# Kernel tuning notes

Hardware: AMD Instinct MI355X
Metric: run time of the kernel (lower is better)

The kernel has to match this reference:

```python
import jax, jax.numpy as jnp
import numpy as np

B, T, D, H, C = 128, 256, 256, 1024, 10


def setup_inputs() -> dict:
    key = jax.random.key(0)
    ks = jax.random.split(key, 11)
    std = 1.0 / T  # matches nn.init.normal_(std=1/seq_length)
    inp = {
        'x':   jax.random.normal(ks[0], (B, T, D), dtype=jnp.float32),
        'Wfx': jax.random.normal(ks[1], (D, H), dtype=jnp.float32) * std,
        'Wix': jax.random.normal(ks[2], (D, H), dtype=jnp.float32) * std,
        'Wgx': jax.random.normal(ks[3], (D, H), dtype=jnp.float32) * std,
        'Wox': jax.random.normal(ks[4], (D, H), dtype=jnp.float32) * std,
        'Wfh': jax.random.normal(ks[5], (H, H), dtype=jnp.float32) * std,
        'Wih': jax.random.normal(ks[6], (H, H), dtype=jnp.float32) * std,
        'Wgh': jax.random.normal(ks[7], (H, H), dtype=jnp.float32) * std,
        'Woh': jax.random.normal(ks[8], (H, H), dtype=jnp.float32) * std,
        'bf':  jnp.zeros((H,), jnp.float32),
        'bi':  jnp.zeros((H,), jnp.float32),
        'bg':  jnp.zeros((H,), jnp.float32),
        'bo':  jnp.zeros((H,), jnp.float32),
        'Wph': jax.random.normal(ks[9], (H, C), dtype=jnp.float32) * std,
        'bp':  jnp.zeros((C,), jnp.float32),
    }
    return inp


def reference(x, Wfx, Wix, Wgx, Wox, Wfh, Wih, Wgh, Woh, bf, bi, bg, bo, Wph, bp):
    b, t, d = x.shape
    h = Wfh.shape[0]
    # Fuse the 4 input-side and 4 hidden-side matmuls into two big GEMMs per step
    Wx = jnp.concatenate([Wfx, Wix, Wgx, Wox], axis=1)  # [D, 4H]
    Wh = jnp.concatenate([Wfh, Wih, Wgh, Woh], axis=1)  # [H, 4H]
    bb = jnp.concatenate([bf, bi, bg, bo])              # [4H]

    # Precompute all input projections in one batched GEMM: [T, B, 4H]
    xg = jnp.einsum('btd,dk->tbk', x, Wx) + bb

    def step(carry, xgt):
        hs, cs = carry
        gates = xgt + hs @ Wh  # [B, 4H]
        f = jax.nn.sigmoid(gates[:, 0 * h:1 * h])
        i = jax.nn.sigmoid(gates[:, 1 * h:2 * h])
        g = jnp.tanh(gates[:, 2 * h:3 * h])
        o = jax.nn.sigmoid(gates[:, 3 * h:4 * h])
        cs = g * i + cs * f
        hs = jnp.tanh(cs) * o
        return (hs, cs), None

    h0 = jnp.zeros((b, h), x.dtype)
    c0 = jnp.zeros((b, h), x.dtype)
    (hT, _), _ = jax.lax.scan(step, (h0, c0), xg)
    return hT @ Wph + bp
```

## Files before the change

### kernel.cpp

```cpp
#include <hip/hip_runtime.h>
#include <math.h>


#define BB 128
#define TT 256
#define DD 256
#define HH 1024
#define NKT 40
#define KHT 20
#define PFA 4
#define PFB 5

typedef __bf16 bf16x8 __attribute__((ext_vector_type(8)));
typedef float  f32x4  __attribute__((ext_vector_type(4)));
typedef unsigned short u16;
typedef u16 u16x8 __attribute__((ext_vector_type(8)));

__device__ __forceinline__ u16 f2bf(float f){
  unsigned u = __builtin_bit_cast(unsigned, f);
  u += 0x7fffu + ((u >> 16) & 1u);
  return (u16)(u >> 16);
}
__device__ __forceinline__ float bf2f(u16 b){
  unsigned u = ((unsigned)b) << 16;
  return __builtin_bit_cast(float, u);
}
__device__ __forceinline__ float sigm(float x){
  return 1.f / (1.f + __expf(-x));
}
__device__ __forceinline__ float tanh_fast(float x){
  return 2.f / (1.f + __expf(-2.f * x)) - 1.f;
}
__device__ __forceinline__ int swzb(int slot){
  return slot ^ ((slot >> 6) & 7) ^ (((slot >> 4) & 3) << 1);
}

__global__ void prep_wpack(const float* __restrict__ Wfx, const float* __restrict__ Wix,
                           const float* __restrict__ Wgx, const float* __restrict__ Wox,
                           const float* __restrict__ Wfh, const float* __restrict__ Wih,
                           const float* __restrict__ Wgh, const float* __restrict__ Woh,
                           u16* __restrict__ Wpack){
  int id = blockIdx.x * 256 + threadIdx.x;
  int lane = id & 63;
  int kt = (id >> 6) % NKT;
  int ct = id / (64 * NKT);
  int col = ct * 16 + (lane & 15);
  int g = col >> 10, n = col & 1023;
  int kbase = kt * 32 + (lane >> 4) * 8;
  const float* Wx = (g==0) ? Wfx : (g==1) ? Wix : (g==2) ? Wgx : Wox;
  const float* Wh = (g==0) ? Wfh : (g==1) ? Wih : (g==2) ? Wgh : Woh;
  u16x8 v;
  #pragma unroll
  for (int j = 0; j < 8; ++j){
    int k = kbase + j;
    float f = (k < DD) ? Wx[k * HH + n] : Wh[(k - DD) * HH + n];
    v[j] = f2bf(f);
  }
  *(u16x8*)(Wpack + (size_t)id * 8) = v;
}

__global__ void prep_xT(const float* __restrict__ x, u16* __restrict__ xT){
  int id = blockIdx.x * 256 + threadIdx.x;
  int t = id >> 12;
  int b = (id >> 5) & 127;
  int d0 = (id & 31) * 8;
  const float* src = x + ((size_t)b * TT + t) * DD + d0;
  u16x8 v;
  #pragma unroll
  for (int j = 0; j < 8; ++j) v[j] = f2bf(src[j]);
  *(u16x8*)(xT + (size_t)id * 8) = v;
}

__global__ __launch_bounds__(512) void lstm_step(
    const u16* __restrict__ xTt,
    const u16* __restrict__ Wpack,
    const u16* __restrict__ hin,
    u16* __restrict__ hout,
    float* __restrict__ cbuf,
    const float* __restrict__ bfv, const float* __restrict__ biv,
    const float* __restrict__ bgv, const float* __restrict__ bov){
  __shared__ u16x8 As4[NKT * 64];
  __shared__ float gLds[16][132];
  __shared__ float pLds[16][132];
  const int tid = threadIdx.x;
  const int n0 = blockIdx.x * 32;
  const int m0 = blockIdx.y * 16;

  const int crow = tid >> 5, cnn = tid & 31;
  const int gi = (m0 + crow) * HH + n0 + cnn;
  const float cprev = cbuf[gi];

  const int w = tid >> 6, lane = tid & 63, cr = lane & 15, q4 = lane >> 4;
  const int g  = w & 3;
  const int kh = w >> 2;
  const int ktBeg = kh * KHT;

  const size_t ct0 = (size_t)(g * 64 + blockIdx.x * 2);
  const u16x8* Wp = (const u16x8*)Wpack;
  const u16x8* wq0 = Wp + ct0 * NKT * 64 + lane;
  const u16x8* wq1 = wq0 + NKT * 64;

  u16x8 aP[PFA], b0P[PFB], b1P[PFB];
  #pragma unroll
  for (int i = 0; i < PFB; ++i){
    b0P[i] = wq0[(size_t)(ktBeg + i) * 64];
    b1P[i] = wq1[(size_t)(ktBeg + i) * 64];
  }

  #pragma unroll
  for (int it = 0; it < 10; ++it){
    int ch = tid + it * 256;
    ch = tid + it * 512;
    if (it >= 5) break;
    int m = ch / 160;
    int k0 = (ch - m * 160) * 8;
    const u16* src = (k0 < DD) ? (xTt + (m0 + m) * DD + k0)
                               : (hin + (m0 + m) * HH + (k0 - DD));
    u16x8 val = *(const u16x8*)src;
    int kt = k0 >> 5, q = (k0 >> 3) & 3;
    As4[swzb(kt * 64 + 16 * q + m)] = val;
  }
  __syncthreads();

  #pragma unroll
  for (int i = 0; i < PFA; ++i) aP[i] = As4[swzb((ktBeg + i) * 64 + lane)];

  f32x4 acc0 = {0.f, 0.f, 0.f, 0.f}, acc1 = {0.f, 0.f, 0.f, 0.f};
  #pragma unroll
  for (int kt = 0; kt < KHT; ++kt){
    u16x8 ac = aP[kt % PFA], b0 = b0P[kt % PFB], b1 = b1P[kt % PFB];
    if (kt + PFA < KHT)
      aP[kt % PFA] = As4[swzb((ktBeg + kt + PFA) * 64 + lane)];
    if (kt + PFB < KHT){
      b0P[kt % PFB] = wq0[(size_t)(ktBeg + kt + PFB) * 64];
      b1P[kt % PFB] = wq1[(size_t)(ktBeg + kt + PFB) * 64];
    }
    acc0 = __builtin_amdgcn_mfma_f32_16x16x32_bf16(__builtin_bit_cast(bf16x8, ac),
             __builtin_bit_cast(bf16x8, b0), acc0, 0, 0, 0);
    acc1 = __builtin_amdgcn_mfma_f32_16x16x32_bf16(__builtin_bit_cast(bf16x8, ac),
             __builtin_bit_cast(bf16x8, b1), acc1, 0, 0, 0);
  }

  if (kh){
    #pragma unroll
    for (int r = 0; r < 4; ++r){
      pLds[q4 * 4 + r][g * 32 + cr]      = acc0[r];
      pLds[q4 * 4 + r][g * 32 + 16 + cr] = acc1[r];
    }
  }
  __syncthreads();
  if (!kh){
    const float* bptr = (g==0) ? bfv : (g==1) ? biv : (g==2) ? bgv : bov;
    float bias0 = bptr[n0 + cr], bias1 = bptr[n0 + 16 + cr];
    #pragma unroll
    for (int r = 0; r < 4; ++r){
      gLds[q4 * 4 + r][g * 32 + cr] =
          acc0[r] + pLds[q4 * 4 + r][g * 32 + cr] + bias0;
      gLds[q4 * 4 + r][g * 32 + 16 + cr] =
          acc1[r] + pLds[q4 * 4 + r][g * 32 + 16 + cr] + bias1;
    }
  }
  __syncthreads();

  {
    float fp = gLds[crow][cnn],      ip = gLds[crow][32 + cnn];
    float gp = gLds[crow][64 + cnn], op = gLds[crow][96 + cnn];
    float fs = sigm(fp);
    float is = sigm(ip);
    float gs = tanh_fast(gp);
    float os = sigm(op);
    float cn = gs * is + cprev * fs;
    cbuf[gi] = cn;
    hout[gi] = f2bf(tanh_fast(cn) * os);
  }
}

__global__ void final_proj(const u16* __restrict__ h, const float* __restrict__ Wph,
                           const float* __restrict__ bp, float* __restrict__ out){
  __shared__ float red[10][256];
  int b = blockIdx.x, tid = threadIdx.x;
  float p[10];
  #pragma unroll
  for (int c = 0; c < 10; ++c) p[c] = 0.f;
  for (int k = tid; k < HH; k += 256){
    float hv = bf2f(h[b * HH + k]);
    const float* wr = Wph + (size_t)k * 10;
    #pragma unroll
    for (int c = 0; c < 10; ++c) p[c] += hv * wr[c];
  }
  #pragma unroll
  for (int c = 0; c < 10; ++c) red[c][tid] = p[c];
  __syncthreads();
  for (int s = 128; s > 0; s >>= 1){
    if (tid < s){
      #pragma unroll
      for (int c = 0; c < 10; ++c) red[c][tid] += red[c][tid + s];
    }
    __syncthreads();
  }
  if (tid < 10) out[b * 10 + tid] = red[tid][0] + bp[tid];
}

extern "C" void kernel_launch(void* const* d_in, const int* in_sizes, int n_in,
                              void* d_out, int out_size, void* d_ws, size_t ws_size,
                              hipStream_t stream){
  (void)in_sizes; (void)n_in; (void)out_size; (void)ws_size;
  const float* x   = (const float*)d_in[0];
  const float* Wfx = (const float*)d_in[1];
  const float* Wix = (const float*)d_in[2];
  const float* Wgx = (const float*)d_in[3];
  const float* Wox = (const float*)d_in[4];
  const float* Wfh = (const float*)d_in[5];
  const float* Wih = (const float*)d_in[6];
  const float* Wgh = (const float*)d_in[7];
  const float* Woh = (const float*)d_in[8];
  const float* bfv = (const float*)d_in[9];
  const float* biv = (const float*)d_in[10];
  const float* bgv = (const float*)d_in[11];
  const float* bov = (const float*)d_in[12];
  const float* Wph = (const float*)d_in[13];
  const float* bp  = (const float*)d_in[14];

  char* ws = (char*)d_ws;
  u16*  Wpack = (u16*)ws;
  u16*  xT    = (u16*)(ws + 10485760);
  u16*  h0    = (u16*)(ws + 27262976);
  u16*  h1    = (u16*)(ws + 27525120);
  float* cb   = (float*)(ws + 27787264);

  prep_wpack<<<2560, 256, 0, stream>>>(Wfx, Wix, Wgx, Wox, Wfh, Wih, Wgh, Woh, Wpack);
  prep_xT<<<4096, 256, 0, stream>>>(x, xT);
  hipMemsetAsync(h0, 0, 262144, stream);
  hipMemsetAsync(cb, 0, 524288, stream);

  for (int t = 0; t < TT; ++t){
    const u16* hin  = (t & 1) ? h1 : h0;
    u16*       hout = (t & 1) ? h0 : h1;
    lstm_step<<<dim3(32, 8), 512, 0, stream>>>(xT + (size_t)t * BB * DD, Wpack,
                                               hin, hout, cb, bfv, biv, bgv, bov);
  }
  final_proj<<<128, 256, 0, stream>>>(h0, Wph, bp, (float*)d_out);
}
```

Before: 1.951 ms.

## Double batch rows per block to reuse weight fragments across two MFMA tiles

Each step block now processes 32 batch rows instead of 16, loading each weight fragment once and using it for two MFMA tiles, which halves the grid size. The split-K reduction writes both halves to separate LDS buffers and sums them in the gate epilogue, dropping one barrier. The weight prefetch depth is raised. This cuts global weight traffic per step but leaves fewer blocks to cover the GPU's compute units and raises per-block LDS and register use.

```diff
diff --git a/kernel.cpp b/kernel.cpp
--- a/kernel.cpp
+++ b/kernel.cpp
@@ -9,7 +9,7 @@
 #define NKT 40
 #define KHT 20
 #define PFA 4
-#define PFB 5
+#define PFB 8
 
 typedef __bf16 bf16x8 __attribute__((ext_vector_type(8)));
 typedef float  f32x4  __attribute__((ext_vector_type(4)));
@@ -71,7 +71,7 @@
   *(u16x8*)(xT + (size_t)id * 8) = v;
 }
 
-__global__ __launch_bounds__(512) void lstm_step(
+__global__ __launch_bounds__(512) void lstm_step3(
     const u16* __restrict__ xTt,
     const u16* __restrict__ Wpack,
     const u16* __restrict__ hin,
@@ -79,16 +79,20 @@
     float* __restrict__ cbuf,
     const float* __restrict__ bfv, const float* __restrict__ biv,
     const float* __restrict__ bgv, const float* __restrict__ bov){
-  __shared__ u16x8 As4[NKT * 64];
-  __shared__ float gLds[16][132];
-  __shared__ float pLds[16][132];
+  __shared__ u16x8 AsLo[NKT * 64];
+  __shared__ u16x8 AsHi[NKT * 64];
+  __shared__ float pLds0[32][132];
+  __shared__ float pLds1[32][132];
   const int tid = threadIdx.x;
   const int n0 = blockIdx.x * 32;
-  const int m0 = blockIdx.y * 16;
-
-  const int crow = tid >> 5, cnn = tid & 31;
-  const int gi = (m0 + crow) * HH + n0 + cnn;
-  const float cprev = cbuf[gi];
+  const int m0 = blockIdx.y * 32;
+
+  const int crow0 = tid >> 5,        cnn0 = tid & 31;
+  const int crow1 = (tid + 512) >> 5, cnn1 = cnn0;
+  const int gi0 = (m0 + crow0) * HH + n0 + cnn0;
+  const int gi1 = (m0 + crow1) * HH + n0 + cnn1;
+  const float cprev0 = cbuf[gi0];
+  const float cprev1 = cbuf[gi1];
 
   const int w = tid >> 6, lane = tid & 63, cr = lane & 15, q4 = lane >> 4;
   const int g  = w & 3;
@@ -100,7 +104,7 @@
   const u16x8* wq0 = Wp + ct0 * NKT * 64 + lane;
   const u16x8* wq1 = wq0 + NKT * 64;
 
-  u16x8 aP[PFA], b0P[PFB], b1P[PFB];
+  u16x8 b0P[PFB], b1P[PFB];
   #pragma unroll
   for (int i = 0; i < PFB; ++i){
     b0P[i] = wq0[(size_t)(ktBeg + i) * 64];
@@ -108,70 +112,98 @@
   }
 
   #pragma unroll
-  for (int it = 0; it < 10; ++it){
-    int ch = tid + it * 256;
-    ch = tid + it * 512;
-    if (it >= 5) break;
+  for (int it = 0; it < 5; ++it){
+    int ch = tid + it * 512;
     int m = ch / 160;
     int k0 = (ch - m * 160) * 8;
     const u16* src = (k0 < DD) ? (xTt + (m0 + m) * DD + k0)
                                : (hin + (m0 + m) * HH + (k0 - DD));
     u16x8 val = *(const u16x8*)src;
     int kt = k0 >> 5, q = (k0 >> 3) & 3;
-    As4[swzb(kt * 64 + 16 * q + m)] = val;
+    AsLo[swzb(kt * 64 + 16 * q + m)] = val;
+  }
+  #pragma unroll
+  for (int it = 0; it < 5; ++it){
+    int ch = tid + it * 512;
+    int m = ch / 160;
+    int k0 = (ch - m * 160) * 8;
+    const u16* src = (k0 < DD) ? (xTt + (m0 + 16 + m) * DD + k0)
+                               : (hin + (m0 + 16 + m) * HH + (k0 - DD));
+    u16x8 val = *(const u16x8*)src;
+    int kt = k0 >> 5, q = (k0 >> 3) & 3;
+    AsHi[swzb(kt * 64 + 16 * q + m)] = val;
   }
   __syncthreads();
 
-  #pragma unroll
-  for (int i = 0; i < PFA; ++i) aP[i] = As4[swzb((ktBeg + i) * 64 + lane)];
-
-  f32x4 acc0 = {0.f, 0.f, 0.f, 0.f}, acc1 = {0.f, 0.f, 0.f, 0.f};
+  u16x8 aLoP[PFA], aHiP[PFA];
+  #pragma unroll
+  for (int i = 0; i < PFA; ++i){
+    aLoP[i] = AsLo[swzb((ktBeg + i) * 64 + lane)];
+    aHiP[i] = AsHi[swzb((ktBeg + i) * 64 + lane)];
+  }
+
+  f32x4 aL0 = {0.f,0.f,0.f,0.f}, aL1 = {0.f,0.f,0.f,0.f};
+  f32x4 aH0 = {0.f,0.f,0.f,0.f}, aH1 = {0.f,0.f,0.f,0.f};
   #pragma unroll
   for (int kt = 0; kt < KHT; ++kt){
-    u16x8 ac = aP[kt % PFA], b0 = b0P[kt % PFB], b1 = b1P[kt % PFB];
-    if (kt + PFA < KHT)
-      aP[kt % PFA] = As4[swzb((ktBeg + kt + PFA) * 64 + lane)];
+    u16x8 alo = aLoP[kt & (PFA - 1)], ahi = aHiP[kt & (PFA - 1)];
+    u16x8 b0  = b0P[kt & (PFB - 1)],  b1  = b1P[kt & (PFB - 1)];
+    if (kt + PFA < KHT){
+      aLoP[kt & (PFA - 1)] = AsLo[swzb((ktBeg + kt + PFA) * 64 + lane)];
+      aHiP[kt & (PFA - 1)] = AsHi[swzb((ktBeg + kt + PFA) * 64 + lane)];
+    }
     if (kt + PFB < KHT){
-      b0P[kt % PFB] = wq0[(size_t)(ktBeg + kt + PFB) * 64];
-      b1P[kt % PFB] = wq1[(size_t)(ktBeg + kt + PFB) * 64];
-    }
-    acc0 = __builtin_amdgcn_mfma_f32_16x16x32_bf16(__builtin_bit_cast(bf16x8, ac),
-             __builtin_bit_cast(bf16x8, b0), acc0, 0, 0, 0);
-    acc1 = __builtin_amdgcn_mfma_f32_16x16x32_bf16(__builtin_bit_cast(bf16x8, ac),
-             __builtin_bit_cast(bf16x8, b1), acc1, 0, 0, 0);
-  }
-
-  if (kh){
+      b0P[kt & (PFB - 1)] = wq0[(size_t)(ktBeg + kt + PFB) * 64];
+      b1P[kt & (PFB - 1)] = wq1[(size_t)(ktBeg + kt + PFB) * 64];
+    }
+    aL0 = __builtin_amdgcn_mfma_f32_16x16x32_bf16(__builtin_bit_cast(bf16x8, alo),
+            __builtin_bit_cast(bf16x8, b0), aL0, 0, 0, 0);
+    aL1 = __builtin_amdgcn_mfma_f32_16x16x32_bf16(__builtin_bit_cast(bf16x8, alo),
+            __builtin_bit_cast(bf16x8, b1), aL1, 0, 0, 0);
+    aH0 = __builtin_amdgcn_mfma_f32_16x16x32_bf16(__builtin_bit_cast(bf16x8, ahi),
+            __builtin_bit_cast(bf16x8, b0), aH0, 0, 0, 0);
+    aH1 = __builtin_amdgcn_mfma_f32_16x16x32_bf16(__builtin_bit_cast(bf16x8, ahi),
+            __builtin_bit_cast(bf16x8, b1), aH1, 0, 0, 0);
+  }
+
+  if (!kh){
+    const float* bptr = (g==0) ? bfv : (g==1) ? biv : (g==2) ? bgv : bov;
+    const float bias0 = bptr[n0 + cr], bias1 = bptr[n0 + 16 + cr];
     #pragma unroll
     for (int r = 0; r < 4; ++r){
-      pLds[q4 * 4 + r][g * 32 + cr]      = acc0[r];
-      pLds[q4 * 4 + r][g * 32 + 16 + cr] = acc1[r];
-    }
-  }
-  __syncthreads();
-  if (!kh){
-    const float* bptr = (g==0) ? bfv : (g==1) ? biv : (g==2) ? bgv : bov;
-    float bias0 = bptr[n0 + cr], bias1 = bptr[n0 + 16 + cr];
+      pLds0[q4 * 4 + r][g * 32 + cr]           = aL0[r] + bias0;
+      pLds0[q4 * 4 + r][g * 32 + 16 + cr]      = aL1[r] + bias1;
+      pLds0[16 + q4 * 4 + r][g * 32 + cr]      = aH0[r] + bias0;
+      pLds0[16 + q4 * 4 + r][g * 32 + 16 + cr] = aH1[r] + bias1;
+    }
+  } else {
     #pragma unroll
     for (int r = 0; r < 4; ++r){
-      gLds[q4 * 4 + r][g * 32 + cr] =
-          acc0[r] + pLds[q4 * 4 + r][g * 32 + cr] + bias0;
-      gLds[q4 * 4 + r][g * 32 + 16 + cr] =
-          acc1[r] + pLds[q4 * 4 + r][g * 32 + 16 + cr] + bias1;
+      pLds1[q4 * 4 + r][g * 32 + cr]           = aL0[r];
+      pLds1[q4 * 4 + r][g * 32 + 16 + cr]      = aL1[r];
+      pLds1[16 + q4 * 4 + r][g * 32 + cr]      = aH0[r];
+      pLds1[16 + q4 * 4 + r][g * 32 + 16 + cr] = aH1[r];
     }
   }
   __syncthreads();
 
   {
-    float fp = gLds[crow][cnn],      ip = gLds[crow][32 + cnn];
-    float gp = gLds[crow][64 + cnn], op = gLds[crow][96 + cnn];
-    float fs = sigm(fp);
-    float is = sigm(ip);
-    float gs = tanh_fast(gp);
-    float os = sigm(op);
-    float cn = gs * is + cprev * fs;
-    cbuf[gi] = cn;
-    hout[gi] = f2bf(tanh_fast(cn) * os);
+    float fp = pLds0[crow0][cnn0]      + pLds1[crow0][cnn0];
+    float ip = pLds0[crow0][32 + cnn0] + pLds1[crow0][32 + cnn0];
+    float gp = pLds0[crow0][64 + cnn0] + pLds1[crow0][64 + cnn0];
+    float op = pLds0[crow0][96 + cnn0] + pLds1[crow0][96 + cnn0];
+    float cn = tanh_fast(gp) * sigm(ip) + cprev0 * sigm(fp);
+    cbuf[gi0] = cn;
+    hout[gi0] = f2bf(tanh_fast(cn) * sigm(op));
+  }
+  {
+    float fp = pLds0[crow1][cnn1]      + pLds1[crow1][cnn1];
+    float ip = pLds0[crow1][32 + cnn1] + pLds1[crow1][32 + cnn1];
+    float gp = pLds0[crow1][64 + cnn1] + pLds1[crow1][64 + cnn1];
+    float op = pLds0[crow1][96 + cnn1] + pLds1[crow1][96 + cnn1];
+    float cn = tanh_fast(gp) * sigm(ip) + cprev1 * sigm(fp);
+    cbuf[gi1] = cn;
+    hout[gi1] = f2bf(tanh_fast(cn) * sigm(op));
   }
 }
 
@@ -236,8 +268,8 @@
   for (int t = 0; t < TT; ++t){
     const u16* hin  = (t & 1) ? h1 : h0;
     u16*       hout = (t & 1) ? h0 : h1;
-    lstm_step<<<dim3(32, 8), 512, 0, stream>>>(xT + (size_t)t * BB * DD, Wpack,
-                                               hin, hout, cb, bfv, biv, bgv, bov);
+    lstm_step3<<<dim3(32, 4), 512, 0, stream>>>(xT + (size_t)t * BB * DD, Wpack,
+                                                hin, hout, cb, bfv, biv, bgv, bov);
   }
   final_proj<<<128, 256, 0, stream>>>(h0, Wph, bp, (float*)d_out);
 }
```

Result: slower. 2.361 ms (+21.0%).
